# Kernel optimization log

Hardware: AMD Instinct MI355X
Metric: run time of the kernel (lower is better)

## Reference

```python
import jax, jax.numpy as jnp
import numpy as np

B, T, D = 4, 256, 1024
E, DL, TOPK, H = 16, 64, 2, 4


def setup_inputs() -> dict:
    key = jax.random.key(0)
    ks = jax.random.split(key, 12)
    n = lambda k, s: (0.02 * jax.random.normal(k, s)).astype(jnp.float32)
    return dict(
        x=jax.random.normal(ks[0], (B, T, D), dtype=jnp.float32),
        w_down=n(ks[1], (E * DL, D)),
        pos_embed=n(ks[2], (1, E, DL)),
        gp_w=n(ks[3], (DL, D)), gp_b=jnp.zeros((DL,), jnp.float32),
        attn_in_w=n(ks[4], (3 * DL, DL)), attn_in_b=jnp.zeros((3 * DL,), jnp.float32),
        attn_out_w=n(ks[5], (DL, DL)), attn_out_b=jnp.zeros((DL,), jnp.float32),
        ln_w=jnp.ones((DL,), jnp.float32), ln_b=jnp.zeros((DL,), jnp.float32),
        ls_w=n(ks[6], (1, DL)), ls_b=jnp.zeros((1,), jnp.float32),
        g1_w=n(ks[7], (2 * DL, DL)), g1_b=jnp.zeros((2 * DL,), jnp.float32),
        g2_w=n(ks[8], (E, 2 * DL)), g2_b=jnp.zeros((E,), jnp.float32),
        w_up=n(ks[9], (E, DL, D)),
    )


def reference(x, w_down, pos_embed, gp_w, gp_b, attn_in_w, attn_in_b,
              attn_out_w, attn_out_b, ln_w, ln_b, ls_w, ls_b,
              g1_w, g1_b, g2_w, g2_b, w_up):
    Bq, Tq, Dm = x.shape
    N = Bq * Tq
    xf = x.reshape(N, Dm)
    # per-token per-expert low-rank features [N, E, DL]
    ef = (xf @ w_down.T).reshape(N, E, DL)
    # global context per batch element -> [B, DL]
    gctx = x.mean(axis=1) @ gp_w.T + gp_b
    gtok = jnp.repeat(gctx, Tq, axis=0)[:, None, :]  # [N, 1, DL]
    seq = jnp.concatenate([gtok, ef + pos_embed], axis=1)  # [N, E+1, DL]
    # tiny multihead self-attention over E+1 tokens, eval mode (no dropout)
    qkv = seq @ attn_in_w.T + attn_in_b
    q, k, v = jnp.split(qkv, 3, axis=-1)
    hd = DL // H
    sh = lambda t: t.reshape(N, E + 1, H, hd).transpose(0, 2, 1, 3)
    q, k, v = sh(q), sh(k), sh(v)
    scores = jnp.einsum('nhqd,nhkd->nhqk', q, k) / np.float32(np.sqrt(hd))
    attn = jax.nn.softmax(scores, axis=-1)
    ctx = jnp.einsum('nhqk,nhkd->nhqd', attn, v).transpose(0, 2, 1, 3).reshape(N, E + 1, DL)
    attn_out = ctx @ attn_out_w.T + attn_out_b
    h = attn_out + seq
    mu = h.mean(-1, keepdims=True)
    var = h.var(-1, keepdims=True)
    hn = (h - mu) / jnp.sqrt(var + 1e-5) * ln_w + ln_b
    refined = hn[:, 1:, :]  # drop global token -> [N, E, DL]
    local_logits = (refined @ ls_w.T + ls_b)[..., 0]  # [N, E]
    gb = jax.nn.gelu(gctx @ g1_w.T + g1_b, approximate=False) @ g2_w.T + g2_b  # [B, E]
    logits = local_logits + jnp.repeat(gb, Tq, axis=0)
    probs = jax.nn.softmax(logits, axis=-1)
    tw, ti = jax.lax.top_k(probs, TOPK)
    tw = tw / tw.sum(-1, keepdims=True)
    sel = jnp.take_along_axis(ef, ti[..., None], axis=1)  # [N, K, DL]
    act = jax.nn.gelu(sel, approximate=False)
    # gather per-token expert up-projections and batched vec-mat
    eo = jnp.einsum('nkd,nkdm->nkm', act, w_up[ti])  # [N, K, D]
    out = (eo * tw[..., None]).sum(axis=1).reshape(Bq, Tq, Dm)
    mean_prob = probs.mean(axis=0)
    one_hot = jnp.zeros_like(probs).at[jnp.arange(N)[:, None], ti].set(1.0)
    aux_loss = E * jnp.sum(mean_prob * one_hot.mean(axis=0))
    return out, aux_loss
```

## Files before the change

### kernel.cpp

```cpp
#include <hip/hip_runtime.h>
#include <math.h>

#define NB 4
#define TT 256
#define DMODEL 1024
#define NE 16
#define DLQ 64
#define NH 4
#define HD 16
#define SEQL 17
#define NTOK 1024

static constexpr size_t WS_EF    = 0;
static constexpr size_t WS_AH    = 1048576;
static constexpr size_t WS_AL    = 1572864;
static constexpr size_t WS_BH    = 2097152;
static constexpr size_t WS_BL    = 2621440;
static constexpr size_t WS_P1    = 3145728;
static constexpr size_t WS_ACT   = 4194304;
static constexpr size_t WS_AIWFH = 4259840;
static constexpr size_t WS_AIWFL = 4265984;
static constexpr size_t WS_AOWFH = 4272128;
static constexpr size_t WS_AOWFL = 4274176;
static constexpr size_t WS_PR    = 4308992;
static constexpr size_t WS_TI    = 4325376;
static constexpr size_t WS_GCTX  = 4326400;
static constexpr size_t WS_GB    = 4326656;
static constexpr size_t WS_GPH   = 4400128;
static constexpr size_t WS_GPL   = 4432896;
static constexpr size_t WS_GPX0  = 4465664;
static constexpr size_t WS_GPX1  = 4531200;

typedef __attribute__((ext_vector_type(8))) short short8;
typedef __attribute__((ext_vector_type(4))) float f32x4;

__device__ __forceinline__ float gelu_exact(float x) {
    return 0.5f * x * (1.0f + erff(x * 0.70710678118654752f));
}

__device__ __forceinline__ unsigned short f2bf(float f) {
    unsigned int u = __float_as_uint(f);
    unsigned int r = (u + 0x7fffu + ((u >> 16) & 1u)) >> 16;
    return (unsigned short)r;
}
__device__ __forceinline__ float bf2f(unsigned short h) {
    return __uint_as_float(((unsigned int)h) << 16);
}

#define DPP_ADD(v, ctrl) { int _m = __builtin_amdgcn_update_dpp(0, __float_as_int(v), ctrl, 0xF, 0xF, true); \
                           v += __int_as_float(_m); }
__device__ __forceinline__ float rsum16(float v) {
    DPP_ADD(v, 0x128);
    DPP_ADD(v, 0x124);
    DPP_ADD(v, 0x122);
    DPP_ADD(v, 0x121);
    return v;
}
__device__ __forceinline__ float rsum64(float v) {
    v = rsum16(v);
    v += __shfl_xor(v, 16);
    v += __shfl_xor(v, 32);
    return v;
}

__global__ __launch_bounds__(256) void k_prep(const float* __restrict__ x,
                                              const float* __restrict__ wdn,
                                              const float* __restrict__ gp_w,
                                              const float* __restrict__ aiw,
                                              const float* __restrict__ aow,
                                              float* __restrict__ ws) {
    int bi = blockIdx.x;
    int tid = threadIdx.x;
    if (bi < 1024) {
        int which = bi >> 9;
        int t = (bi & 511) * 256 + tid;
        int row = t >> 7;
        int col0 = (t & 127) * 8;
        const float* src = which ? wdn : x;
        unsigned short* hp = (unsigned short*)(ws + (which ? WS_BH : WS_AH));
        unsigned short* lp = (unsigned short*)(ws + (which ? WS_BL : WS_AL));
        float4 v0 = *(const float4*)(src + (size_t)row * DMODEL + col0);
        float4 v1 = *(const float4*)(src + (size_t)row * DMODEL + col0 + 4);
        float vv[8] = {v0.x, v0.y, v0.z, v0.w, v1.x, v1.y, v1.z, v1.w};
        unsigned short h8[8], l8[8];
#pragma unroll
        for (int j = 0; j < 8; ++j) {
            h8[j] = f2bf(vv[j]);
            l8[j] = f2bf(vv[j] - bf2f(h8[j]));
        }
        int nb = row >> 6, kb = col0 >> 6;
        int st = (row & 63) >> 4;
        int ks = (col0 & 63) >> 5;
        int ln = (row & 15) + (((col0 >> 3) & 3) << 4);
        size_t off = (size_t)(nb * 16 + kb) * 4096 + st * 1024 + ks * 512 + ln * 8;
        *(short8*)(hp + off) = *(short8*)h8;
        *(short8*)(lp + off) = *(short8*)l8;
    } else if (bi < 1056) {
        int t = (bi - 1024) * 256 + tid;
        int row = t >> 7;
        int col0 = (t & 127) * 8;
        unsigned short* hp = (unsigned short*)(ws + WS_GPH);
        unsigned short* lp = (unsigned short*)(ws + WS_GPL);
        float4 v0 = *(const float4*)(gp_w + (size_t)row * DMODEL + col0);
        float4 v1 = *(const float4*)(gp_w + (size_t)row * DMODEL + col0 + 4);
        float vv[8] = {v0.x, v0.y, v0.z, v0.w, v1.x, v1.y, v1.z, v1.w};
        unsigned short h8[8], l8[8];
#pragma unroll
        for (int j = 0; j < 8; ++j) {
            h8[j] = f2bf(vv[j]);
            l8[j] = f2bf(vv[j] - bf2f(h8[j]));
        }
        int kb = col0 >> 6;
        int st = row >> 4;
        int ks = (col0 & 63) >> 5;
        int ln = (row & 15) + (((col0 >> 3) & 3) << 4);
        size_t off = (size_t)kb * 4096 + st * 1024 + ks * 512 + ln * 8;
        *(short8*)(hp + off) = *(short8*)h8;
        *(short8*)(lp + off) = *(short8*)l8;
    } else {
        unsigned short* fh = (unsigned short*)(ws + WS_AIWFH);
        unsigned short* fl = (unsigned short*)(ws + WS_AIWFL);
        for (int idx = tid; idx < 12 * 2 * 64; idx += 256) {
            int nt = idx >> 7, kf = (idx >> 6) & 1, l = idx & 63;
            int row = nt * 16 + (l & 15);
            int k = kf * 32 + ((l >> 4) << 3);
            const float* src = aiw + (size_t)row * DLQ + k;
            unsigned short h8[8], l8[8];
#pragma unroll
            for (int j = 0; j < 8; ++j) {
                h8[j] = f2bf(src[j]);
                l8[j] = f2bf(src[j] - bf2f(h8[j]));
            }
            size_t off = (size_t)(nt * 2 + kf) * 512 + l * 8;
            *(short8*)(fh + off) = *(short8*)h8;
            *(short8*)(fl + off) = *(short8*)l8;
        }
        unsigned short* gh = (unsigned short*)(ws + WS_AOWFH);
        unsigned short* gl = (unsigned short*)(ws + WS_AOWFL);
        for (int idx = tid; idx < 4 * 2 * 64; idx += 256) {
            int nt = idx >> 7, kf = (idx >> 6) & 1, l = idx & 63;
            int row = nt * 16 + (l & 15);
            int k = kf * 32 + ((l >> 4) << 3);
            const float* src = aow + (size_t)row * DLQ + k;
            unsigned short h8[8], l8[8];
#pragma unroll
            for (int j = 0; j < 8; ++j) {
                h8[j] = f2bf(src[j]);
                l8[j] = f2bf(src[j] - bf2f(h8[j]));
            }
            size_t off = (size_t)(nt * 2 + kf) * 512 + l * 8;
            *(short8*)(gh + off) = *(short8*)h8;
            *(short8*)(gl + off) = *(short8*)l8;
        }
    }
}

__global__ __launch_bounds__(256) void k_ef_mfma(float* __restrict__ ws) {
    __shared__ __attribute__((aligned(16))) unsigned short smem[16384];
    int tid = threadIdx.x;
    int bi = blockIdx.x;

    int nb, mb, kz;
    bool gp = bi >= 512;
    if (gp) {
        int idx = bi - 512;
        nb = idx & 15;
        kz = idx >> 4;
        mb = 0;
    } else {
        int xcd = bi & 7;
        int g   = bi >> 3;
        kz  = g >> 5;
        int rem = g & 31;
        nb  = (xcd >> 1) * 4 + (rem >> 3);
        mb  = (xcd & 1) * 8 + (rem & 7);
    }

    const unsigned short* AhP = (const unsigned short*)(ws + WS_AH);
    const unsigned short* AlP = (const unsigned short*)(ws + WS_AL);
    const unsigned short* BhP = gp ? (const unsigned short*)(ws + WS_GPH)
                                   : (const unsigned short*)(ws + WS_BH);
    const unsigned short* BlP = gp ? (const unsigned short*)(ws + WS_GPL)
                                   : (const unsigned short*)(ws + WS_BL);
    int w = tid >> 6, l = tid & 63;
    int wn = (w >> 1) * 32, wm = (w & 1) * 32;
    int stA = wn >> 4, stB = wm >> 4;
    f32x4 acc00 = {0.f, 0.f, 0.f, 0.f}, acc01 = acc00, acc10 = acc00, acc11 = acc00;

    for (int it = 0; it < 8; ++it) {
        int kb = kz * 8 + it;
        const char* srcs[4] = {
            (const char*)(AhP + (size_t)(nb * 16 + kb) * 4096),
            (const char*)(AlP + (size_t)(nb * 16 + kb) * 4096),
            (const char*)(BhP + (size_t)(mb * 16 + kb) * 4096),
            (const char*)(BlP + (size_t)(mb * 16 + kb) * 4096)};
#pragma unroll
        for (int p = 0; p < 4; ++p) {
#pragma unroll
            for (int h = 0; h < 2; ++h) {
                __builtin_amdgcn_global_load_lds(
                    (const __attribute__((address_space(1))) void*)(srcs[p] + h * 4096 + tid * 16),
                    (__attribute__((address_space(3))) void*)((char*)smem + p * 8192 + h * 4096 + tid * 16),
                    16, 0, 0);
            }
        }
        __syncthreads();
        const unsigned short* Ah = smem;
        const unsigned short* Al = smem + 4096;
        const unsigned short* Bh = smem + 8192;
        const unsigned short* Bl = smem + 12288;
#pragma unroll
        for (int ks = 0; ks < 2; ++ks) {
            short8 ah0 = *(const short8*)(Ah + (stA + 0) * 1024 + ks * 512 + l * 8);
            short8 ah1 = *(const short8*)(Ah + (stA + 1) * 1024 + ks * 512 + l * 8);
            short8 al0 = *(const short8*)(Al + (stA + 0) * 1024 + ks * 512 + l * 8);
            short8 al1 = *(const short8*)(Al + (stA + 1) * 1024 + ks * 512 + l * 8);
            short8 bh0 = *(const short8*)(Bh + (stB + 0) * 1024 + ks * 512 + l * 8);
            short8 bh1 = *(const short8*)(Bh + (stB + 1) * 1024 + ks * 512 + l * 8);
            short8 bl0 = *(const short8*)(Bl + (stB + 0) * 1024 + ks * 512 + l * 8);
            short8 bl1 = *(const short8*)(Bl + (stB + 1) * 1024 + ks * 512 + l * 8);
            acc00 = __builtin_amdgcn_mfma_f32_16x16x32_bf16(ah0, bh0, acc00, 0, 0, 0);
            acc00 = __builtin_amdgcn_mfma_f32_16x16x32_bf16(al0, bh0, acc00, 0, 0, 0);
            acc00 = __builtin_amdgcn_mfma_f32_16x16x32_bf16(ah0, bl0, acc00, 0, 0, 0);
            acc01 = __builtin_amdgcn_mfma_f32_16x16x32_bf16(ah0, bh1, acc01, 0, 0, 0);
            acc01 = __builtin_amdgcn_mfma_f32_16x16x32_bf16(al0, bh1, acc01, 0, 0, 0);
            acc01 = __builtin_amdgcn_mfma_f32_16x16x32_bf16(ah0, bl1, acc01, 0, 0, 0);
            acc10 = __builtin_amdgcn_mfma_f32_16x16x32_bf16(ah1, bh0, acc10, 0, 0, 0);
            acc10 = __builtin_amdgcn_mfma_f32_16x16x32_bf16(al1, bh0, acc10, 0, 0, 0);
            acc10 = __builtin_amdgcn_mfma_f32_16x16x32_bf16(ah1, bl0, acc10, 0, 0, 0);
            acc11 = __builtin_amdgcn_mfma_f32_16x16x32_bf16(ah1, bh1, acc11, 0, 0, 0);
            acc11 = __builtin_amdgcn_mfma_f32_16x16x32_bf16(al1, bh1, acc11, 0, 0, 0);
            acc11 = __builtin_amdgcn_mfma_f32_16x16x32_bf16(ah1, bl1, acc11, 0, 0, 0);
        }
        __syncthreads();
    }
    int cr = (l >> 4) * 4, cc = l & 15;
    int n0 = nb * 64;
    float* P;
    size_t rstride;
    int m0;
    if (gp) {
        P = ws + (kz == 0 ? WS_GPX0 : WS_GPX1);
        rstride = 64;
        m0 = 0;
    } else {
        P = ws + (kz == 0 ? WS_EF : WS_P1);
        rstride = DMODEL;
        m0 = mb * 64;
    }
#pragma unroll
    for (int r = 0; r < 4; ++r) {
        P[(size_t)(n0 + wn + cr + r) * rstride + (m0 + wm + cc)]           = acc00[r];
        P[(size_t)(n0 + wn + cr + r) * rstride + (m0 + wm + 16 + cc)]      = acc01[r];
        P[(size_t)(n0 + wn + 16 + cr + r) * rstride + (m0 + wm + cc)]      = acc10[r];
        P[(size_t)(n0 + wn + 16 + cr + r) * rstride + (m0 + wm + 16 + cc)] = acc11[r];
    }
}

__global__ __launch_bounds__(256) void k_gctx(const float* __restrict__ gp_b,
                                              const float* __restrict__ g1_w,
                                              const float* __restrict__ g1_b,
                                              const float* __restrict__ g2_w,
                                              const float* __restrict__ g2_b,
                                              float* __restrict__ ws) {
    __shared__ float part[4][DLQ];
    __shared__ float gc[DLQ];
    __shared__ float gb1[128];
    int b = blockIdx.x;
    int tid = threadIdx.x;
    int wv = tid >> 6, l = tid & 63;
    {
        const float* g0 = ws + WS_GPX0 + (size_t)(b * 256 + wv * 64) * 64 + l;
        const float* g1p = ws + WS_GPX1 + (size_t)(b * 256 + wv * 64) * 64 + l;
        float s = 0.f;
#pragma unroll 8
        for (int t = 0; t < 64; ++t) s += g0[t * 64] + g1p[t * 64];
        part[wv][l] = s;
    }
    __syncthreads();
    if (wv == 0) {
        float v = (part[0][l] + part[1][l] + part[2][l] + part[3][l]) * (1.0f / TT) + gp_b[l];
        gc[l] = v;
        ws[WS_GCTX + b * DLQ + l] = v;
    }
    __syncthreads();
    {
        float gcl = gc[l];
        for (int rq = 0; rq < 8; ++rq) {
            int o = wv * 32 + rq * 4;
            float s[4];
#pragma unroll
            for (int r = 0; r < 4; ++r) s[r] = gcl * g1_w[(size_t)(o + r) * DLQ + l];
#pragma unroll
            for (int r = 0; r < 4; ++r) s[r] = rsum64(s[r]);
            if (l == 0) {
#pragma unroll
                for (int r = 0; r < 4; ++r) gb1[o + r] = gelu_exact(s[r] + g1_b[o + r]);
            }
        }
    }
    __syncthreads();
    {
        float v0 = gb1[l * 2], v1 = gb1[l * 2 + 1];
        int o = wv * 4;
        float s[4];
#pragma unroll
        for (int r = 0; r < 4; ++r)
            s[r] = v0 * g2_w[(size_t)(o + r) * 128 + l * 2] +
                   v1 * g2_w[(size_t)(o + r) * 128 + l * 2 + 1];
#pragma unroll
        for (int r = 0; r < 4; ++r) s[r] = rsum64(s[r]);
        if (l == 0) {
#pragma unroll
            for (int r = 0; r < 4; ++r) ws[WS_GB + b * NE + o + r] = s[r] + g2_b[o + r];
        }
    }
}

__global__ __launch_bounds__(128) void k_attn2(const float* __restrict__ pos_embed,
                                               const float* __restrict__ attn_in_b,
                                               const float* __restrict__ attn_out_b,
                                               const float* __restrict__ ln_w,
                                               const float* __restrict__ ln_b,
                                               const float* __restrict__ ls_w,
                                               const float* __restrict__ ls_b,
                                               float* __restrict__ ws) {
    int n = blockIdx.x;
    int w = threadIdx.x >> 6;
    int l = threadIdx.x & 63;
    int b = n >> 8;

    __shared__ float qkv[SEQL * 200];
    __shared__ __attribute__((aligned(16))) char ubuf[8192];
    __shared__ __attribute__((aligned(16))) unsigned short ctxH[1024];
    __shared__ __attribute__((aligned(16))) unsigned short ctxL[1024];
    __shared__ float lgv_sh[NE];
    unsigned short* sH = (unsigned short*)ubuf;
    unsigned short* sL = (unsigned short*)(ubuf + 4096);
    float* ao = (float*)ubuf;

    float seqc[SEQL];
    {
        const float* efp0 = ws + WS_EF + (size_t)n * DMODEL;
        const float* efp1 = ws + WS_P1 + (size_t)n * DMODEL;
        float gcv = ws[WS_GCTX + b * DLQ + l];
#pragma unroll
        for (int i = 0; i < SEQL; ++i) {
            float s = (i == 0) ? gcv
                               : efp0[(i - 1) * DLQ + l] + efp1[(i - 1) * DLQ + l] +
                                 pos_embed[(i - 1) * DLQ + l];
            seqc[i] = s;
            int lo_r = w * 9, hi_r = w * 9 + 8;
            if (i >= lo_r && i <= hi_r && i < SEQL) {
                unsigned short hs = f2bf(s);
                unsigned short lsv = f2bf(s - bf2f(hs));
                int mt = i >> 4;
                int ls = (i & 15) + (((l >> 3) & 3) << 4);
                int kf = l >> 5;
                int j = l & 7;
                size_t off = (size_t)(mt * 2 + kf) * 512 + ls * 8 + j;
                sH[off] = hs;
                sL[off] = lsv;
            }
        }
    }
    __syncthreads();

    {
        const unsigned short* fh = (const unsigned short*)(ws + WS_AIWFH);
        const unsigned short* fl = (const unsigned short*)(ws + WS_AIWFL);
        f32x4 acc[6][2];
#pragma unroll
        for (int t = 0; t < 6; ++t)
#pragma unroll
            for (int m = 0; m < 2; ++m) acc[t][m] = (f32x4){0.f, 0.f, 0.f, 0.f};
#pragma unroll
        for (int kf = 0; kf < 2; ++kf) {
            short8 ah0 = *(const short8*)(sH + (0 * 2 + kf) * 512 + l * 8);
            short8 ah1 = *(const short8*)(sH + (1 * 2 + kf) * 512 + l * 8);
            short8 al0 = *(const short8*)(sL + (0 * 2 + kf) * 512 + l * 8);
            short8 al1 = *(const short8*)(sL + (1 * 2 + kf) * 512 + l * 8);
#pragma unroll
            for (int t = 0; t < 6; ++t) {
                int nt = w * 6 + t;
                short8 bh = *(const short8*)(fh + (size_t)(nt * 2 + kf) * 512 + l * 8);
                short8 bl = *(const short8*)(fl + (size_t)(nt * 2 + kf) * 512 + l * 8);
                acc[t][0] = __builtin_amdgcn_mfma_f32_16x16x32_bf16(ah0, bh, acc[t][0], 0, 0, 0);
                acc[t][0] = __builtin_amdgcn_mfma_f32_16x16x32_bf16(al0, bh, acc[t][0], 0, 0, 0);
                acc[t][0] = __builtin_amdgcn_mfma_f32_16x16x32_bf16(ah0, bl, acc[t][0], 0, 0, 0);
                acc[t][1] = __builtin_amdgcn_mfma_f32_16x16x32_bf16(ah1, bh, acc[t][1], 0, 0, 0);
                acc[t][1] = __builtin_amdgcn_mfma_f32_16x16x32_bf16(al1, bh, acc[t][1], 0, 0, 0);
                acc[t][1] = __builtin_amdgcn_mfma_f32_16x16x32_bf16(ah1, bl, acc[t][1], 0, 0, 0);
            }
        }
#pragma unroll
        for (int t = 0; t < 6; ++t) {
            int col = (w * 6 + t) * 16 + (l & 15);
            float bias = attn_in_b[col];
#pragma unroll
            for (int r = 0; r < 4; ++r) {
                int row = (l >> 4) * 4 + r;
                qkv[row * 200 + col] = acc[t][0][r] + bias;
            }
            if ((l >> 4) == 0) qkv[16 * 200 + col] = acc[t][1][0] + bias;
        }
    }
    __syncthreads();

    {
        int g = l >> 4;
        float kc[SEQL], vc[SEQL];
#pragma unroll
        for (int j = 0; j < SEQL; ++j) {
            kc[j] = qkv[j * 200 + 64 + g * 16 + (l & 15)];
            vc[j] = qkv[j * 200 + 128 + l];
        }
        for (int i = w * 8 + 1; i <= w * 8 + 8; ++i) {
            float qi = qkv[i * 200 + g * 16 + (l & 15)];
            float sj[SEQL];
#pragma unroll
            for (int j = 0; j < SEQL; ++j) {
                sj[j] = rsum16(qi * kc[j]) * 0.25f;
            }
            float m = sj[0];
#pragma unroll
            for (int j = 1; j < SEQL; ++j) m = fmaxf(m, sj[j]);
            float ssum = 0.f;
#pragma unroll
            for (int j = 0; j < SEQL; ++j) { sj[j] = __expf(sj[j] - m); ssum += sj[j]; }
            float inv = 1.f / ssum;
            float c = 0.f;
#pragma unroll
            for (int j = 0; j < SEQL; ++j) c += sj[j] * vc[j];
            c *= inv;
            unsigned short ch = f2bf(c);
            unsigned short cl = f2bf(c - bf2f(ch));
            int ls = ((i - 1) & 15) + (((l >> 3) & 3) << 4);
            int kf = l >> 5;
            int j2 = l & 7;
            size_t off = (size_t)kf * 512 + ls * 8 + j2;
            ctxH[off] = ch;
            ctxL[off] = cl;
        }
    }
    __syncthreads();

    {
        const unsigned short* gh = (const unsigned short*)(ws + WS_AOWFH);
        const unsigned short* gl = (const unsigned short*)(ws + WS_AOWFL);
        f32x4 acc[2];
        acc[0] = (f32x4){0.f, 0.f, 0.f, 0.f};
        acc[1] = acc[0];
#pragma unroll
        for (int kf = 0; kf < 2; ++kf) {
            short8 ah = *(const short8*)(ctxH + kf * 512 + l * 8);
            short8 al = *(const short8*)(ctxL + kf * 512 + l * 8);
#pragma unroll
            for (int t = 0; t < 2; ++t) {
                int nt = w * 2 + t;
                short8 bh = *(const short8*)(gh + (size_t)(nt * 2 + kf) * 512 + l * 8);
                short8 bl = *(const short8*)(gl + (size_t)(nt * 2 + kf) * 512 + l * 8);
                acc[t] = __builtin_amdgcn_mfma_f32_16x16x32_bf16(ah, bh, acc[t], 0, 0, 0);
                acc[t] = __builtin_amdgcn_mfma_f32_16x16x32_bf16(al, bh, acc[t], 0, 0, 0);
                acc[t] = __builtin_amdgcn_mfma_f32_16x16x32_bf16(ah, bl, acc[t], 0, 0, 0);
            }
        }
        __syncthreads();
#pragma unroll
        for (int t = 0; t < 2; ++t) {
            int col = (w * 2 + t) * 16 + (l & 15);
            float bias = attn_out_b[col];
#pragma unroll
            for (int r = 0; r < 4; ++r) {
                int row = (l >> 4) * 4 + r;
                ao[row * 72 + col] = acc[t][r] + bias;
            }
        }
    }
    __syncthreads();

    float rs[SEQL];
#pragma unroll
    for (int i = 1; i < SEQL; ++i) rs[i] = seqc[i] + ao[(i - 1) * 72 + l];

    float c1 = ln_w[l] * ls_w[l];
    float c1sum = rsum64(c1);
    float c0sum = rsum64(ln_b[l] * ls_w[l]);
    float lsb0 = ls_b[0];
#pragma unroll
    for (int ee = 0; ee < 8; ++ee) {
        int e = w * 8 + ee;
        float x = rs[e + 1];
        float s1 = rsum64(x);
        float s2 = rsum64(x * x);
        float s3 = rsum64(x * c1);
        float mu = s1 * (1.0f / DLQ);
        float var = s2 * (1.0f / DLQ) - mu * mu;
        float rstd = rsqrtf(var + 1e-5f);
        float lgv = rstd * (s3 - mu * c1sum) + c0sum + lsb0 + ws[WS_GB + b * NE + e];
        if (l == 0) lgv_sh[e] = lgv;
    }
    __syncthreads();

    if (w == 0) {
        float p[NE];
        float lgv[NE];
#pragma unroll
        for (int e = 0; e < NE; ++e) lgv[e] = lgv_sh[e];
        float m = lgv[0];
#pragma unroll
        for (int e = 1; e < NE; ++e) m = fmaxf(m, lgv[e]);
        float ssum = 0.f;
#pragma unroll
        for (int e = 0; e < NE; ++e) { p[e] = __expf(lgv[e] - m); ssum += p[e]; }
        float inv = 1.f / ssum;
#pragma unroll
        for (int e = 0; e < NE; ++e) p[e] *= inv;
        int t0 = 0; float b0 = p[0];
#pragma unroll
        for (int e = 1; e < NE; ++e) if (p[e] > b0) { b0 = p[e]; t0 = e; }
        int t1 = -1; float b1 = -1.f;
#pragma unroll
        for (int e = 0; e < NE; ++e) if (e != t0 && p[e] > b1) { b1 = p[e]; t1 = e; }

        float sw = b0 + b1;
        float tw0 = b0 / sw, tw1 = b1 / sw;
        unsigned short* actp = (unsigned short*)(ws + WS_ACT);
        float efv0 = ws[WS_EF + (size_t)n * DMODEL + t0 * DLQ + l] +
                     ws[WS_P1 + (size_t)n * DMODEL + t0 * DLQ + l];
        float efv1 = ws[WS_EF + (size_t)n * DMODEL + t1 * DLQ + l] +
                     ws[WS_P1 + (size_t)n * DMODEL + t1 * DLQ + l];
        actp[(size_t)(n * 2 + 0) * 64 + l] = f2bf(gelu_exact(efv0) * tw0);
        actp[(size_t)(n * 2 + 1) * 64 + l] = f2bf(gelu_exact(efv1) * tw1);
        if (l == 0) {
#pragma unroll
            for (int e = 0; e < NE; ++e) ws[WS_PR + (size_t)n * NE + e] = p[e];
            ((int*)(ws + WS_TI))[n] = t0 | (t1 << 8);
        }
    }
}

__global__ __launch_bounds__(256) void k_moe_gemm(const float* __restrict__ w_up,
                                                  float* __restrict__ ws,
                                                  float* __restrict__ out) {
    __shared__ int lst[2048];
    __shared__ int lcnt;
    __shared__ float wsum[4][NE];
    __shared__ int hist[NE];
    int tid = threadIdx.x;
    int wv = tid >> 6, l = tid & 63;

    if (blockIdx.x == NE) {
        if (blockIdx.y != 0) return;
        if (tid < NE) hist[tid] = 0;
        __syncthreads();
        {
            const int* tip = (const int*)(ws + WS_TI);
#pragma unroll
            for (int c = 0; c < 4; ++c) {
                int pk = tip[tid * 4 + c];
                atomicAdd(&hist[pk & 0xff], 1);
                atomicAdd(&hist[(pk >> 8) & 0xff], 1);
            }
        }
        float p[NE];
#pragma unroll
        for (int e = 0; e < NE; ++e) p[e] = 0.f;
        const float* pr = ws + WS_PR + (size_t)tid * 64;
#pragma unroll
        for (int r = 0; r < 4; ++r)
#pragma unroll
            for (int q = 0; q < 4; ++q) {
                float4 v = *(const float4*)(pr + r * 16 + q * 4);
                p[q * 4 + 0] += v.x; p[q * 4 + 1] += v.y;
                p[q * 4 + 2] += v.z; p[q * 4 + 3] += v.w;
            }
#pragma unroll
        for (int e = 0; e < NE; ++e) p[e] = rsum64(p[e]);
        if (l == 0) {
#pragma unroll
            for (int e = 0; e < NE; ++e) wsum[wv][e] = p[e];
        }
        __syncthreads();
        if (tid == 0) {
            float s = 0.f;
#pragma unroll
            for (int e = 0; e < NE; ++e) {
                float sp = wsum[0][e] + wsum[1][e] + wsum[2][e] + wsum[3][e];
                s += sp * (float)hist[e];
            }
            out[(size_t)NTOK * DMODEL] = (float)NE * s / ((float)NTOK * (float)NTOK);
        }
        return;
    }

    int e = blockIdx.x, ct = blockIdx.y;
    if (tid == 0) lcnt = 0;
    __syncthreads();
    {
        const int* tip = (const int*)(ws + WS_TI);
#pragma unroll
        for (int c = 0; c < 4; ++c) {
            int tok = wv * 256 + c * 64 + l;
            int pk = tip[tok];
            bool m1 = ((pk >> 8) & 0xff) == e;
            bool m = ((pk & 0xff) == e) || m1;
            unsigned long long mask = __ballot(m);
            int base = 0;
            if (l == 0 && mask) base = atomicAdd(&lcnt, __popcll(mask));
            base = __shfl(base, 0);
            if (m) {
                int pos = base + __popcll(mask & ((1ull << l) - 1ull));
                lst[pos] = tok * 2 + (m1 ? 1 : 0);
            }
        }
    }
    __syncthreads();
    int cnt = lcnt;
    if (cnt == 0) return;

    int col = ct * 64 + wv * 16 + (l & 15);
    int kb = (l >> 4) * 8;
    const float* wue = w_up + (size_t)e * DLQ * DMODEL + col;
    unsigned short b0v[8], b1v[8];
#pragma unroll
    for (int j = 0; j < 8; ++j) {
        b0v[j] = f2bf(wue[(size_t)(kb + j) * DMODEL]);
        b1v[j] = f2bf(wue[(size_t)(kb + 32 + j) * DMODEL]);
    }
    short8 bf0 = *(short8*)b0v;
    short8 bf1 = *(short8*)b1v;

    const unsigned short* actp = (const unsigned short*)(ws + WS_ACT);
    int cr = (l >> 4) * 4;

    for (int mt = 0; mt < cnt; mt += 16) {
        int row = mt + (l & 15);
        short8 a0 = {0, 0, 0, 0, 0, 0, 0, 0};
        short8 a1 = {0, 0, 0, 0, 0, 0, 0, 0};
        if (row < cnt) {
            int pk = lst[row];
            a0 = *(const short8*)(actp + (size_t)pk * 64 + kb);
            a1 = *(const short8*)(actp + (size_t)pk * 64 + 32 + kb);
        }
        f32x4 acc = {0.f, 0.f, 0.f, 0.f};
        acc = __builtin_amdgcn_mfma_f32_16x16x32_bf16(a0, bf0, acc, 0, 0, 0);
        acc = __builtin_amdgcn_mfma_f32_16x16x32_bf16(a1, bf1, acc, 0, 0, 0);
#pragma unroll
        for (int r = 0; r < 4; ++r) {
            int rr = mt + cr + r;
            if (rr < cnt) {
                int pk = lst[rr];
                atomicAdd(&out[(size_t)(pk >> 1) * DMODEL + col], acc[r]);
            }
        }
    }
}

extern "C" void kernel_launch(void* const* d_in, const int* in_sizes, int n_in,
                              void* d_out, int out_size, void* d_ws, size_t ws_size,
                              hipStream_t stream) {
    const float* x          = (const float*)d_in[0];
    const float* w_down     = (const float*)d_in[1];
    const float* pos_embed  = (const float*)d_in[2];
    const float* gp_w       = (const float*)d_in[3];
    const float* gp_b       = (const float*)d_in[4];
    const float* attn_in_w  = (const float*)d_in[5];
    const float* attn_in_b  = (const float*)d_in[6];
    const float* attn_out_w = (const float*)d_in[7];
    const float* attn_out_b = (const float*)d_in[8];
    const float* ln_w       = (const float*)d_in[9];
    const float* ln_b       = (const float*)d_in[10];
    const float* ls_w       = (const float*)d_in[11];
    const float* ls_b       = (const float*)d_in[12];
    const float* g1_w       = (const float*)d_in[13];
    const float* g1_b       = (const float*)d_in[14];
    const float* g2_w       = (const float*)d_in[15];
    const float* g2_b       = (const float*)d_in[16];
    const float* w_up       = (const float*)d_in[17];
    float* ws  = (float*)d_ws;
    float* out = (float*)d_out;

    hipMemsetAsync(out, 0, (size_t)out_size * sizeof(float), stream);
    k_prep<<<1057, 256, 0, stream>>>(x, w_down, gp_w, attn_in_w, attn_out_w, ws);
    k_ef_mfma<<<544, 256, 0, stream>>>(ws);
    k_gctx<<<NB, 256, 0, stream>>>(gp_b, g1_w, g1_b, g2_w, g2_b, ws);
    k_attn2<<<NTOK, 128, 0, stream>>>(pos_embed, attn_in_b, attn_out_b,
                                      ln_w, ln_b, ls_w, ls_b, ws);
    k_moe_gemm<<<dim3(NE + 1, 16), 256, 0, stream>>>(w_up, ws, out);
}
```

Measured before the change: 167.3 us.

## Compute global context as mean-then-project and fold into ef GEMM launch

```diff
diff --git a/kernel.cpp b/kernel.cpp
--- a/kernel.cpp
+++ b/kernel.cpp
@@ -26,10 +26,7 @@
 static constexpr size_t WS_TI    = 4325376;
 static constexpr size_t WS_GCTX  = 4326400;
 static constexpr size_t WS_GB    = 4326656;
-static constexpr size_t WS_GPH   = 4400128;
-static constexpr size_t WS_GPL   = 4432896;
-static constexpr size_t WS_GPX0  = 4465664;
-static constexpr size_t WS_GPX1  = 4531200;
+static constexpr size_t WS_XMEAN = 4465664;
 
 typedef __attribute__((ext_vector_type(8))) short short8;
 typedef __attribute__((ext_vector_type(4))) float f32x4;
@@ -65,7 +62,6 @@
 
 __global__ __launch_bounds__(256) void k_prep(const float* __restrict__ x,
                                               const float* __restrict__ wdn,
-                                              const float* __restrict__ gp_w,
                                               const float* __restrict__ aiw,
                                               const float* __restrict__ aow,
                                               float* __restrict__ ws) {
@@ -82,6 +78,11 @@
         float4 v0 = *(const float4*)(src + (size_t)row * DMODEL + col0);
         float4 v1 = *(const float4*)(src + (size_t)row * DMODEL + col0 + 4);
         float vv[8] = {v0.x, v0.y, v0.z, v0.w, v1.x, v1.y, v1.z, v1.w};
+        if (which == 0) {
+            float* xm = ws + WS_XMEAN + (size_t)(row >> 8) * DMODEL + col0;
+#pragma unroll
+            for (int j = 0; j < 8; ++j) atomicAdd(xm + j, vv[j]);
+        }
         unsigned short h8[8], l8[8];
 #pragma unroll
         for (int j = 0; j < 8; ++j) {
@@ -93,28 +94,6 @@
         int ks = (col0 & 63) >> 5;
         int ln = (row & 15) + (((col0 >> 3) & 3) << 4);
         size_t off = (size_t)(nb * 16 + kb) * 4096 + st * 1024 + ks * 512 + ln * 8;
-        *(short8*)(hp + off) = *(short8*)h8;
-        *(short8*)(lp + off) = *(short8*)l8;
-    } else if (bi < 1056) {
-        int t = (bi - 1024) * 256 + tid;
-        int row = t >> 7;
-        int col0 = (t & 127) * 8;
-        unsigned short* hp = (unsigned short*)(ws + WS_GPH);
-        unsigned short* lp = (unsigned short*)(ws + WS_GPL);
-        float4 v0 = *(const float4*)(gp_w + (size_t)row * DMODEL + col0);
-        float4 v1 = *(const float4*)(gp_w + (size_t)row * DMODEL + col0 + 4);
-        float vv[8] = {v0.x, v0.y, v0.z, v0.w, v1.x, v1.y, v1.z, v1.w};
-        unsigned short h8[8], l8[8];
-#pragma unroll
-        for (int j = 0; j < 8; ++j) {
-            h8[j] = f2bf(vv[j]);
-            l8[j] = f2bf(vv[j] - bf2f(h8[j]));
-        }
-        int kb = col0 >> 6;
-        int st = row >> 4;
-        int ks = (col0 & 63) >> 5;
-        int ln = (row & 15) + (((col0 >> 3) & 3) << 4);
-        size_t off = (size_t)kb * 4096 + st * 1024 + ks * 512 + ln * 8;
         *(short8*)(hp + off) = *(short8*)h8;
         *(short8*)(lp + off) = *(short8*)l8;
     } else {
@@ -155,33 +134,77 @@
     }
 }
 
-__global__ __launch_bounds__(256) void k_ef_mfma(float* __restrict__ ws) {
+__global__ __launch_bounds__(256) void k_ef_mfma(const float* __restrict__ gp_w,
+                                                 const float* __restrict__ gp_b,
+                                                 const float* __restrict__ g1_w,
+                                                 const float* __restrict__ g1_b,
+                                                 const float* __restrict__ g2_w,
+                                                 const float* __restrict__ g2_b,
+                                                 float* __restrict__ ws) {
     __shared__ __attribute__((aligned(16))) unsigned short smem[16384];
     int tid = threadIdx.x;
     int bi = blockIdx.x;
 
-    int nb, mb, kz;
-    bool gp = bi >= 512;
-    if (gp) {
-        int idx = bi - 512;
-        nb = idx & 15;
-        kz = idx >> 4;
-        mb = 0;
-    } else {
-        int xcd = bi & 7;
-        int g   = bi >> 3;
-        kz  = g >> 5;
-        int rem = g & 31;
-        nb  = (xcd >> 1) * 4 + (rem >> 3);
-        mb  = (xcd & 1) * 8 + (rem & 7);
-    }
+    if (bi == 512) {
+        float* gcsh = (float*)smem;
+        int wv = tid >> 6, l = tid & 63;
+        const float* xm = ws + WS_XMEAN + (size_t)wv * DMODEL;
+        const float* gw = gp_w + (size_t)l * DMODEL;
+        float s = 0.f;
+#pragma unroll 4
+        for (int d = 0; d < DMODEL; d += 8) {
+            float4 a0 = *(const float4*)(xm + d);
+            float4 a1 = *(const float4*)(xm + d + 4);
+            float4 b0 = *(const float4*)(gw + d);
+            float4 b1 = *(const float4*)(gw + d + 4);
+            s += a0.x * b0.x + a0.y * b0.y + a0.z * b0.z + a0.w * b0.w
+               + a1.x * b1.x + a1.y * b1.y + a1.z * b1.z + a1.w * b1.w;
+        }
+        float v = s * (1.0f / TT) + gp_b[l];
+        gcsh[wv * DLQ + l] = v;
+        ws[WS_GCTX + wv * DLQ + l] = v;
+        __syncthreads();
+        const float* w0 = g1_w + (size_t)(2 * l) * DLQ;
+        const float* w1 = g1_w + (size_t)(2 * l + 1) * DLQ;
+        float s0 = 0.f, s1 = 0.f;
+#pragma unroll 8
+        for (int c = 0; c < DLQ; ++c) {
+            float g = gcsh[wv * DLQ + c];
+            s0 += g * w0[c];
+            s1 += g * w1[c];
+        }
+        float h0 = gelu_exact(s0 + g1_b[2 * l]);
+        float h1 = gelu_exact(s1 + g1_b[2 * l + 1]);
+#pragma unroll
+        for (int rq = 0; rq < 4; ++rq) {
+            int o = rq * 4;
+            float sr[4];
+#pragma unroll
+            for (int r = 0; r < 4; ++r)
+                sr[r] = h0 * g2_w[(size_t)(o + r) * 128 + 2 * l] +
+                        h1 * g2_w[(size_t)(o + r) * 128 + 2 * l + 1];
+#pragma unroll
+            for (int r = 0; r < 4; ++r) sr[r] = rsum64(sr[r]);
+            if (l == 0) {
+#pragma unroll
+                for (int r = 0; r < 4; ++r)
+                    ws[WS_GB + wv * NE + o + r] = sr[r] + g2_b[o + r];
+            }
+        }
+        return;
+    }
+
+    int xcd = bi & 7;
+    int g   = bi >> 3;
+    int kz  = g >> 5;
+    int rem = g & 31;
+    int nb  = (xcd >> 1) * 4 + (rem >> 3);
+    int mb  = (xcd & 1) * 8 + (rem & 7);
 
     const unsigned short* AhP = (const unsigned short*)(ws + WS_AH);
     const unsigned short* AlP = (const unsigned short*)(ws + WS_AL);
-    const unsigned short* BhP = gp ? (const unsigned short*)(ws + WS_GPH)
-                                   : (const unsigned short*)(ws + WS_BH);
-    const unsigned short* BlP = gp ? (const unsigned short*)(ws + WS_GPL)
-                                   : (const unsigned short*)(ws + WS_BL);
+    const unsigned short* BhP = (const unsigned short*)(ws + WS_BH);
+    const unsigned short* BlP = (const unsigned short*)(ws + WS_BL);
     int w = tid >> 6, l = tid & 63;
     int wn = (w >> 1) * 32, wm = (w & 1) * 32;
     int stA = wn >> 4, stB = wm >> 4;
@@ -236,84 +259,14 @@
     }
     int cr = (l >> 4) * 4, cc = l & 15;
     int n0 = nb * 64;
-    float* P;
-    size_t rstride;
-    int m0;
-    if (gp) {
-        P = ws + (kz == 0 ? WS_GPX0 : WS_GPX1);
-        rstride = 64;
-        m0 = 0;
-    } else {
-        P = ws + (kz == 0 ? WS_EF : WS_P1);
-        rstride = DMODEL;
-        m0 = mb * 64;
-    }
+    float* P = ws + (kz == 0 ? WS_EF : WS_P1);
+    int m0 = mb * 64;
 #pragma unroll
     for (int r = 0; r < 4; ++r) {
-        P[(size_t)(n0 + wn + cr + r) * rstride + (m0 + wm + cc)]           = acc00[r];
-        P[(size_t)(n0 + wn + cr + r) * rstride + (m0 + wm + 16 + cc)]      = acc01[r];
-        P[(size_t)(n0 + wn + 16 + cr + r) * rstride + (m0 + wm + cc)]      = acc10[r];
-        P[(size_t)(n0 + wn + 16 + cr + r) * rstride + (m0 + wm + 16 + cc)] = acc11[r];
-    }
-}
-
-__global__ __launch_bounds__(256) void k_gctx(const float* __restrict__ gp_b,
-                                              const float* __restrict__ g1_w,
-                                              const float* __restrict__ g1_b,
-                                              const float* __restrict__ g2_w,
-                                              const float* __restrict__ g2_b,
-                                              float* __restrict__ ws) {
-    __shared__ float part[4][DLQ];
-    __shared__ float gc[DLQ];
-    __shared__ float gb1[128];
-    int b = blockIdx.x;
-    int tid = threadIdx.x;
-    int wv = tid >> 6, l = tid & 63;
-    {
-        const float* g0 = ws + WS_GPX0 + (size_t)(b * 256 + wv * 64) * 64 + l;
-        const float* g1p = ws + WS_GPX1 + (size_t)(b * 256 + wv * 64) * 64 + l;
-        float s = 0.f;
-#pragma unroll 8
-        for (int t = 0; t < 64; ++t) s += g0[t * 64] + g1p[t * 64];
-        part[wv][l] = s;
-    }
-    __syncthreads();
-    if (wv == 0) {
-        float v = (part[0][l] + part[1][l] + part[2][l] + part[3][l]) * (1.0f / TT) + gp_b[l];
-        gc[l] = v;
-        ws[WS_GCTX + b * DLQ + l] = v;
-    }
-    __syncthreads();
-    {
-        float gcl = gc[l];
-        for (int rq = 0; rq < 8; ++rq) {
-            int o = wv * 32 + rq * 4;
-            float s[4];
-#pragma unroll
-            for (int r = 0; r < 4; ++r) s[r] = gcl * g1_w[(size_t)(o + r) * DLQ + l];
-#pragma unroll
-            for (int r = 0; r < 4; ++r) s[r] = rsum64(s[r]);
-            if (l == 0) {
-#pragma unroll
-                for (int r = 0; r < 4; ++r) gb1[o + r] = gelu_exact(s[r] + g1_b[o + r]);
-            }
-        }
-    }
-    __syncthreads();
-    {
-        float v0 = gb1[l * 2], v1 = gb1[l * 2 + 1];
-        int o = wv * 4;
-        float s[4];
-#pragma unroll
-        for (int r = 0; r < 4; ++r)
-            s[r] = v0 * g2_w[(size_t)(o + r) * 128 + l * 2] +
-                   v1 * g2_w[(size_t)(o + r) * 128 + l * 2 + 1];
-#pragma unroll
-        for (int r = 0; r < 4; ++r) s[r] = rsum64(s[r]);
-        if (l == 0) {
-#pragma unroll
-            for (int r = 0; r < 4; ++r) ws[WS_GB + b * NE + o + r] = s[r] + g2_b[o + r];
-        }
+        P[(size_t)(n0 + wn + cr + r) * DMODEL + (m0 + wm + cc)]           = acc00[r];
+        P[(size_t)(n0 + wn + cr + r) * DMODEL + (m0 + wm + 16 + cc)]      = acc01[r];
+        P[(size_t)(n0 + wn + 16 + cr + r) * DMODEL + (m0 + wm + cc)]      = acc10[r];
+        P[(size_t)(n0 + wn + 16 + cr + r) * DMODEL + (m0 + wm + 16 + cc)] = acc11[r];
     }
 }
 
@@ -682,9 +635,9 @@
     float* out = (float*)d_out;
 
     hipMemsetAsync(out, 0, (size_t)out_size * sizeof(float), stream);
-    k_prep<<<1057, 256, 0, stream>>>(x, w_down, gp_w, attn_in_w, attn_out_w, ws);
-    k_ef_mfma<<<544, 256, 0, stream>>>(ws);
-    k_gctx<<<NB, 256, 0, stream>>>(gp_b, g1_w, g1_b, g2_w, g2_b, ws);
+    hipMemsetAsync(ws + WS_XMEAN, 0, (size_t)NB * DMODEL * sizeof(float), stream);
+    k_prep<<<1025, 256, 0, stream>>>(x, w_down, attn_in_w, attn_out_w, ws);
+    k_ef_mfma<<<513, 256, 0, stream>>>(gp_w, gp_b, g1_w, g1_b, g2_w, g2_b, ws);
     k_attn2<<<NTOK, 128, 0, stream>>>(pos_embed, attn_in_b, attn_out_b,
                                       ln_w, ln_b, ls_w, ls_b, ws);
     k_moe_gemm<<<dim3(NE + 1, 16), 256, 0, stream>>>(w_up, ws, out);
```

After: 256.5 us. +53.3%, slower.
